# Optimization experiments

Hardware: AMD Instinct MI355X
Metric: run time of the kernel (lower is better)

## Reference

```python
import jax, jax.numpy as jnp
import numpy as np

B, S, IN, H, L = 512, 1024, 64, 32, 4


def setup_inputs() -> dict:
    key = jax.random.key(0)
    ks = jax.random.split(key, 9)
    s = 1.0 / np.sqrt(H)  # PyTorch RNN/Linear init scale
    u = lambda k, shape: jax.random.uniform(k, shape, jnp.float32, -s, s)
    return {
        "x": jax.random.normal(ks[0], (B, S, IN), jnp.float32),
        "h_state": jnp.zeros((L, B, H), jnp.float32),
        "W_ih0": u(ks[1], (H, IN)),          # layer 0 input weights
        "W_ih_rest": u(ks[2], (L - 1, H, H)),  # layers 1..3 input weights
        "W_hh": u(ks[3], (L, H, H)),
        "b_ih": u(ks[4], (L, H)),
        "b_hh": u(ks[5], (L, H)),
        "fc_w": u(ks[6], (1, H)),
        "fc_b": u(ks[7], (1,)),
    }


def _rnn_layer(seq_sbf, h0, W_ih, W_hh, b):
    # seq_sbf: [S, B, F]; vanilla RNN: h_t = tanh(x_t W_ih^T + h_{t-1} W_hh^T + b)
    def step(h, x_t):
        h = jnp.tanh(x_t @ W_ih.T + h @ W_hh.T + b)
        return h, h
    return jax.lax.scan(step, h0, seq_sbf)


def reference(x, h_state, W_ih0, W_ih_rest, W_hh, b_ih, b_hh, fc_w, fc_b):
    seq = jnp.swapaxes(x, 0, 1)  # [S, B, IN]
    h_finals = []
    for l in range(L):  # fixed small layer count
        W_ih = W_ih0 if l == 0 else W_ih_rest[l - 1]
        h_last, seq = _rnn_layer(seq, h_state[l], W_ih, W_hh[l], b_ih[l] + b_hh[l])
        h_finals.append(h_last)
    r_out = jnp.swapaxes(seq, 0, 1)                 # [B, S, H]
    logits = (r_out @ fc_w.T + fc_b)[..., 0]        # fused per-timestep Linear -> [B, S]
    probs = jax.nn.softmax(logits, axis=-1)         # nn.Softmax over last (seq) dim
    return probs, jnp.stack(h_finals, axis=0)       # [B,S], [L,B,H]
```

## Files before the change

kernel.cpp:

```cpp
#include <hip/hip_runtime.h>


#define BB 512
#define SS 1024
#define INF 64
#define HH 32
#define LL 4

typedef __fp16 v2h __attribute__((ext_vector_type(2)));

__device__ __forceinline__ v2h bch(unsigned u) { return __builtin_bit_cast(v2h, u); }
__device__ __forceinline__ unsigned bcu(v2h h) { return __builtin_bit_cast(unsigned, h); }

template <int CTRL>
__device__ __forceinline__ float dpp_add(float v) {
  int y = __builtin_amdgcn_update_dpp(0, __float_as_int(v), CTRL, 0xF, 0xF, true);
  return v + __int_as_float(y);
}
template <int CTRL>
__device__ __forceinline__ float dpp_mov(float v) {
  int y = __builtin_amdgcn_update_dpp(0, __float_as_int(v), CTRL, 0xF, 0xF, true);
  return __int_as_float(y);
}

__device__ __forceinline__ float tanh_fast(float a) {
  const float e = __builtin_amdgcn_exp2f(a * 2.885390081777927f);
  const float r = __builtin_amdgcn_rcpf(e + 1.0f);
  return __builtin_fmaf(-2.0f, r, 1.0f);
}

__device__ __forceinline__ float dot16v(const v2h* w, uint4 u0, uint4 u1) {
  float a = 0.f, c = 0.f;
  a = __builtin_amdgcn_fdot2(w[0], bch(u0.x), a, false);
  c = __builtin_amdgcn_fdot2(w[1], bch(u0.y), c, false);
  a = __builtin_amdgcn_fdot2(w[2], bch(u0.z), a, false);
  c = __builtin_amdgcn_fdot2(w[3], bch(u0.w), c, false);
  a = __builtin_amdgcn_fdot2(w[4], bch(u1.x), a, false);
  c = __builtin_amdgcn_fdot2(w[5], bch(u1.y), c, false);
  a = __builtin_amdgcn_fdot2(w[6], bch(u1.z), a, false);
  c = __builtin_amdgcn_fdot2(w[7], bch(u1.w), c, false);
  return a + c;
}

#define BAR() asm volatile("s_waitcnt lgkmcnt(0)\n\ts_barrier" ::: "memory")

__global__ __launch_bounds__(256) void u0_kernel(
    const float* __restrict__ x, const float* __restrict__ W_ih0,
    const float* __restrict__ b_ih, const float* __restrict__ b_hh,
    float* __restrict__ u0) {
  __shared__ float Wl[HH * INF];
  __shared__ float bl[HH];
  const int tid = threadIdx.x;
  {
    const float4* src = (const float4*)W_ih0;
    float4* dst = (float4*)Wl;
    dst[tid] = src[tid];
    dst[tid + 256] = src[tid + 256];
    if (tid < HH) bl[tid] = b_ih[tid] + b_hh[tid];
  }
  __syncthreads();

  const int row = blockIdx.x * 256 + tid;
  const float4* xr = (const float4*)(x + (size_t)row * INF);
  float acc[HH];
#pragma unroll
  for (int u = 0; u < HH; ++u) acc[u] = bl[u];
#pragma unroll 4
  for (int kc = 0; kc < 16; ++kc) {
    const float4 xv = xr[kc];
#pragma unroll
    for (int u = 0; u < HH; ++u) {
      const float4 wv = ((const float4*)Wl)[u * 16 + kc];
      acc[u] += wv.x * xv.x + wv.y * xv.y + wv.z * xv.z + wv.w * xv.w;
    }
  }
  float4* op = (float4*)(u0 + (size_t)row * HH);
#pragma unroll
  for (int j = 0; j < 8; ++j)
    op[j] = make_float4(acc[4 * j], acc[4 * j + 1], acc[4 * j + 2], acc[4 * j + 3]);
}

__global__ __launch_bounds__(256, 2) void rnn_kernel(
    const float* __restrict__ u0g_all, const float* __restrict__ h_state,
    const float* __restrict__ W_ih_rest, const float* __restrict__ W_hh,
    const float* __restrict__ b_ih, const float* __restrict__ b_hh,
    const float* __restrict__ fc_w, const float* __restrict__ fc_b,
    float* __restrict__ out) {
  __shared__ int hb[LL][2][2][16];
  __shared__ float h3f[2][2][32];
  __shared__ float lbuf[64];

  const int tid  = threadIdx.x;
  const int wid  = tid >> 6;
  const int lane = tid & 63;
  const int b    = blockIdx.x;
  const int ks   = lane & 1;
  const int h    = lane >> 1;

  v2h wih[8], whh[8];
  {
    const float2* ph = (const float2*)(W_hh + (size_t)(wid * HH + h) * HH + ks * 16);
#pragma unroll
    for (int j = 0; j < 8; ++j) whh[j] = __builtin_amdgcn_cvt_pkrtz(ph[j].x, ph[j].y);
  }
  float bias = 0.f;
  if (wid > 0) {
    const float2* pi =
        (const float2*)(W_ih_rest + (size_t)((wid - 1) * HH + h) * HH + ks * 16);
#pragma unroll
    for (int j = 0; j < 8; ++j) wih[j] = __builtin_amdgcn_cvt_pkrtz(pi[j].x, pi[j].y);
    bias = b_ih[wid * HH + h] + b_hh[wid * HH + h];
  }
  const float fcwh = fc_w[h] * 0.5f;
  const float fcb  = fc_b[0];

  if (lane < 16) {
    float a = h_state[(size_t)(wid * BB + b) * HH + 2 * lane];
    float c = h_state[(size_t)(wid * BB + b) * HH + 2 * lane + 1];
    hb[wid][(wid + 1) & 1][1][lane] = (int)bcu(__builtin_amdgcn_cvt_pkrtz(a, c));
  }

  const float* ug = u0g_all + (size_t)b * SS * HH;
  float ur[8];
  if (wid == 0) {
#pragma unroll
    for (int i = 0; i < 8; ++i) ur[i] = ug[i * HH + h];
  }
  float* const outrow = out + (size_t)b * SS;
  float* const hfin   = out + (size_t)BB * SS;

  __syncthreads();

  auto ld2 = [&](const int* p, uint4& A, uint4& B) __attribute__((always_inline)) {
    const uint4* q = (const uint4*)p;
    A = q[0]; B = q[1];
  };
  auto store_h = [&](int l, int buf, int slot, float hv) __attribute__((always_inline)) {
    float partner = dpp_mov<0xEE>(hv);
    if ((lane & 3) == 0)
      hb[l][buf][slot][lane >> 2] = (int)bcu(__builtin_amdgcn_cvt_pkrtz(hv, partner));
  };
  auto fcred = [&](float v) __attribute__((always_inline)) {
    v = dpp_add<0x111>(v);
    v = dpp_add<0x112>(v);
    v = dpp_add<0x114>(v);
    v = dpp_add<0x118>(v);
    v = dpp_add<0x142>(v);
    v = dpp_add<0x143>(v);
    return v;
  };

  if (wid == 0) {
    for (int n0 = 0; n0 < 516; n0 += 4) {
#pragma unroll
      for (int j = 0; j < 4; ++j) {
        BAR();
        const int n = n0 + j;
        const int buf = n & 1;
        if (n < 512) {
          uint4 Ha, Hb;
          ld2(&hb[0][buf ^ 1][1][ks * 8], Ha, Hb);
          float acc0 = dot16v(whh, Ha, Hb);
          acc0 = dpp_add<0xB1>(acc0) + ur[2 * j];
          const float hv0 = tanh_fast(acc0);
          store_h(0, buf, 0, hv0);
          uint4 Ga, Gb;
          ld2(&hb[0][buf][0][ks * 8], Ga, Gb);
          float acc1 = dot16v(whh, Ga, Gb);
          acc1 = dpp_add<0xB1>(acc1) + ur[2 * j + 1];
          const float hv1 = tanh_fast(acc1);
          store_h(0, buf, 1, hv1);
          if (n == 511 && ks == 0) hfin[(0 * BB + b) * HH + h] = hv1;
          int ta = 2 * n + 8; ta = ta < SS ? ta : SS - 1;
          int tb = 2 * n + 9; tb = tb < SS ? tb : SS - 1;
          ur[2 * j]     = ug[ta * HH + h];
          ur[2 * j + 1] = ug[tb * HH + h];
        }
        if (n >= 4) {
          const int tf = 2 * n - 7;
          float v0 = fcred(h3f[buf ^ 1][0][h] * fcwh);
          float v1 = fcred(h3f[buf ^ 1][1][h] * fcwh);
          if (lane == 63) {
            lbuf[(tf - 1) & 63] = v0 + fcb;
            lbuf[tf & 63]       = v1 + fcb;
          }
          if ((tf & 63) == 63) {
            float lv = lbuf[lane];
            outrow[tf - 63 + lane] = lv;
          }
        }
      }
    }
  } else if (wid < 3) {
    for (int n0 = 0; n0 < 516; n0 += 4) {
#pragma unroll
      for (int j = 0; j < 4; ++j) {
        BAR();
        const int n = n0 + j;
        const int buf = n & 1;
        if (n >= wid && n < 512 + wid) {
          uint4 I0a, I0b, I1a, I1b, Ha, Hb;
          ld2(&hb[wid - 1][buf ^ 1][0][ks * 8], I0a, I0b);
          ld2(&hb[wid - 1][buf ^ 1][1][ks * 8], I1a, I1b);
          ld2(&hb[wid][buf ^ 1][1][ks * 8], Ha, Hb);
          float acc0 = dot16v(wih, I0a, I0b) + dot16v(whh, Ha, Hb);
          acc0 = dpp_add<0xB1>(acc0) + bias;
          const float hv0 = tanh_fast(acc0);
          store_h(wid, buf, 0, hv0);
          uint4 Ga, Gb;
          ld2(&hb[wid][buf][0][ks * 8], Ga, Gb);
          float acc1 = dot16v(wih, I1a, I1b) + dot16v(whh, Ga, Gb);
          acc1 = dpp_add<0xB1>(acc1) + bias;
          const float hv1 = tanh_fast(acc1);
          store_h(wid, buf, 1, hv1);
          if (n == 511 + wid && ks == 0) hfin[(wid * BB + b) * HH + h] = hv1;
        }
      }
    }
  } else {
    for (int n0 = 0; n0 < 516; n0 += 4) {
#pragma unroll
      for (int j = 0; j < 4; ++j) {
        BAR();
        const int n = n0 + j;
        const int buf = n & 1;
        if (n >= 3 && n < 515) {
          uint4 I0a, I0b, I1a, I1b, Ha, Hb;
          ld2(&hb[2][buf ^ 1][0][ks * 8], I0a, I0b);
          ld2(&hb[2][buf ^ 1][1][ks * 8], I1a, I1b);
          ld2(&hb[3][buf ^ 1][1][ks * 8], Ha, Hb);
          float acc0 = dot16v(wih, I0a, I0b) + dot16v(whh, Ha, Hb);
          acc0 = dpp_add<0xB1>(acc0) + bias;
          const float hv0 = tanh_fast(acc0);
          store_h(3, buf, 0, hv0);
          if (ks == 0) h3f[buf][0][h] = hv0;
          uint4 Ga, Gb;
          ld2(&hb[3][buf][0][ks * 8], Ga, Gb);
          float acc1 = dot16v(wih, I1a, I1b) + dot16v(whh, Ga, Gb);
          acc1 = dpp_add<0xB1>(acc1) + bias;
          const float hv1 = tanh_fast(acc1);
          store_h(3, buf, 1, hv1);
          if (ks == 0) h3f[buf][1][h] = hv1;
          if (n == 514 && ks == 0) hfin[(3 * BB + b) * HH + h] = hv1;
        }
      }
    }
  }
}

__global__ __launch_bounds__(256) void softmax_kernel(float* __restrict__ out) {
  __shared__ float red[8];
  const int row = blockIdx.x;
  float* p = out + (size_t)row * SS;
  const int tid = threadIdx.x;
  float4 v = ((const float4*)p)[tid];
  float m = fmaxf(fmaxf(v.x, v.y), fmaxf(v.z, v.w));
#pragma unroll
  for (int d = 32; d >= 1; d >>= 1) m = fmaxf(m, __shfl_xor(m, d));
  if ((tid & 63) == 0) red[tid >> 6] = m;
  __syncthreads();
  m = fmaxf(fmaxf(red[0], red[1]), fmaxf(red[2], red[3]));
  const float e0 = __expf(v.x - m), e1 = __expf(v.y - m);
  const float e2 = __expf(v.z - m), e3 = __expf(v.w - m);
  float s = (e0 + e1) + (e2 + e3);
#pragma unroll
  for (int d = 32; d >= 1; d >>= 1) s += __shfl_xor(s, d);
  if ((tid & 63) == 0) red[4 + (tid >> 6)] = s;
  __syncthreads();
  s = (red[4] + red[5]) + (red[6] + red[7]);
  const float inv = 1.0f / s;
  float4 o;
  o.x = e0 * inv; o.y = e1 * inv; o.z = e2 * inv; o.w = e3 * inv;
  ((float4*)p)[tid] = o;
}

extern "C" void kernel_launch(void* const* d_in, const int* in_sizes, int n_in,
                              void* d_out, int out_size, void* d_ws, size_t ws_size,
                              hipStream_t stream) {
  const float* x         = (const float*)d_in[0];
  const float* h_state   = (const float*)d_in[1];
  const float* W_ih0     = (const float*)d_in[2];
  const float* W_ih_rest = (const float*)d_in[3];
  const float* W_hh      = (const float*)d_in[4];
  const float* b_ih      = (const float*)d_in[5];
  const float* b_hh      = (const float*)d_in[6];
  const float* fc_w      = (const float*)d_in[7];
  const float* fc_b      = (const float*)d_in[8];
  float* out = (float*)d_out;
  float* u0  = (float*)d_ws;

  hipLaunchKernelGGL(u0_kernel, dim3((BB * SS) / 256), dim3(256), 0, stream,
                     x, W_ih0, b_ih, b_hh, u0);
  hipLaunchKernelGGL(rnn_kernel, dim3(BB), dim3(256), 0, stream,
                     u0, h_state, W_ih_rest, W_hh, b_ih, b_hh, fc_w, fc_b, out);
  hipLaunchKernelGGL(softmax_kernel, dim3(BB), dim3(256), 0, stream, out);
}
```

Measured before the change: 457.0 us.

## Prefetch layer inputs a step early and keep recurrent state in registers

Each layer wave now loads its input from the previous layer one barrier step ahead into a double-buffered register array. Consequently the layer wavefront skew grows from one to two steps per layer, and the loop count, bounds and FC timestep offsets are adjusted to match. The second-slot hidden state is kept in registers (sv) and read right after storing, so the next step's critical path no longer waits on an LDS read. Initial state comes straight from global into registers, and the pre-loop __syncthreads is removed. This shortens the per-step dependency chain between barriers, at the cost of more registers and a few extra pipeline steps.

```diff
diff --git a/kernel.cpp b/kernel.cpp
--- a/kernel.cpp
+++ b/kernel.cpp
@@ -29,16 +29,13 @@
   return __builtin_fmaf(-2.0f, r, 1.0f);
 }
 
-__device__ __forceinline__ float dot16v(const v2h* w, uint4 u0, uint4 u1) {
+__device__ __forceinline__ float dot16p(const v2h* w, const v2h* v) {
   float a = 0.f, c = 0.f;
-  a = __builtin_amdgcn_fdot2(w[0], bch(u0.x), a, false);
-  c = __builtin_amdgcn_fdot2(w[1], bch(u0.y), c, false);
-  a = __builtin_amdgcn_fdot2(w[2], bch(u0.z), a, false);
-  c = __builtin_amdgcn_fdot2(w[3], bch(u0.w), c, false);
-  a = __builtin_amdgcn_fdot2(w[4], bch(u1.x), a, false);
-  c = __builtin_amdgcn_fdot2(w[5], bch(u1.y), c, false);
-  a = __builtin_amdgcn_fdot2(w[6], bch(u1.z), a, false);
-  c = __builtin_amdgcn_fdot2(w[7], bch(u1.w), c, false);
+#pragma unroll
+  for (int j = 0; j < 4; ++j) {
+    a = __builtin_amdgcn_fdot2(w[2 * j + 0], v[2 * j + 0], a, false);
+    c = __builtin_amdgcn_fdot2(w[2 * j + 1], v[2 * j + 1], c, false);
+  }
   return a + c;
 }
 
@@ -114,10 +111,12 @@
   const float fcwh = fc_w[h] * 0.5f;
   const float fcb  = fc_b[0];
 
-  if (lane < 16) {
-    float a = h_state[(size_t)(wid * BB + b) * HH + 2 * lane];
-    float c = h_state[(size_t)(wid * BB + b) * HH + 2 * lane + 1];
-    hb[wid][(wid + 1) & 1][1][lane] = (int)bcu(__builtin_amdgcn_cvt_pkrtz(a, c));
+  v2h sv[8];
+  {
+    const float2* hs = (const float2*)(h_state + (size_t)(wid * BB + b) * HH);
+#pragma unroll
+    for (int j = 0; j < 8; ++j)
+      sv[j] = __builtin_amdgcn_cvt_pkrtz(hs[ks * 8 + j].x, hs[ks * 8 + j].y);
   }
 
   const float* ug = u0g_all + (size_t)b * SS * HH;
@@ -129,11 +128,11 @@
   float* const outrow = out + (size_t)b * SS;
   float* const hfin   = out + (size_t)BB * SS;
 
-  __syncthreads();
-
-  auto ld2 = [&](const int* p, uint4& A, uint4& B) __attribute__((always_inline)) {
+  auto ld8 = [&](const int* p, v2h* v) __attribute__((always_inline)) {
     const uint4* q = (const uint4*)p;
-    A = q[0]; B = q[1];
+    uint4 A = q[0], B = q[1];
+    v[0] = bch(A.x); v[1] = bch(A.y); v[2] = bch(A.z); v[3] = bch(A.w);
+    v[4] = bch(B.x); v[5] = bch(B.y); v[6] = bch(B.z); v[7] = bch(B.w);
   };
   auto store_h = [&](int l, int buf, int slot, float hv) __attribute__((always_inline)) {
     float partner = dpp_mov<0xEE>(hv);
@@ -150,36 +149,43 @@
     return v;
   };
 
+  v2h vi[2][2][8];
+
   if (wid == 0) {
-    for (int n0 = 0; n0 < 516; n0 += 4) {
+    for (int n0 = 0; n0 < 520; n0 += 4) {
 #pragma unroll
       for (int j = 0; j < 4; ++j) {
         BAR();
         const int n = n0 + j;
-        const int buf = n & 1;
-        if (n < 512) {
-          uint4 Ha, Hb;
-          ld2(&hb[0][buf ^ 1][1][ks * 8], Ha, Hb);
-          float acc0 = dot16v(whh, Ha, Hb);
+        const int buf = j & 1;
+        float a0 = 0.f, a1 = 0.f;
+        const bool fc_on = (n >= 7 && n <= 518);
+        if (fc_on) {
+          a0 = h3f[buf ^ 1][0][h];
+          a1 = h3f[buf ^ 1][1][h];
+        }
+        if (n <= 511) {
+          float acc0 = dot16p(whh, sv);
           acc0 = dpp_add<0xB1>(acc0) + ur[2 * j];
           const float hv0 = tanh_fast(acc0);
           store_h(0, buf, 0, hv0);
-          uint4 Ga, Gb;
-          ld2(&hb[0][buf][0][ks * 8], Ga, Gb);
-          float acc1 = dot16v(whh, Ga, Gb);
+          v2h sv0[8];
+          ld8(&hb[0][buf][0][ks * 8], sv0);
+          float acc1 = dot16p(whh, sv0);
           acc1 = dpp_add<0xB1>(acc1) + ur[2 * j + 1];
           const float hv1 = tanh_fast(acc1);
           store_h(0, buf, 1, hv1);
+          ld8(&hb[0][buf][1][ks * 8], sv);
           if (n == 511 && ks == 0) hfin[(0 * BB + b) * HH + h] = hv1;
           int ta = 2 * n + 8; ta = ta < SS ? ta : SS - 1;
           int tb = 2 * n + 9; tb = tb < SS ? tb : SS - 1;
           ur[2 * j]     = ug[ta * HH + h];
           ur[2 * j + 1] = ug[tb * HH + h];
         }
-        if (n >= 4) {
-          const int tf = 2 * n - 7;
-          float v0 = fcred(h3f[buf ^ 1][0][h] * fcwh);
-          float v1 = fcred(h3f[buf ^ 1][1][h] * fcwh);
+        if (fc_on) {
+          const int tf = 2 * n - 13;
+          float v0 = fcred(a0 * fcwh);
+          float v1 = fcred(a1 * fcwh);
           if (lane == 63) {
             lbuf[(tf - 1) & 63] = v0 + fcb;
             lbuf[tf & 63]       = v1 + fcb;
@@ -192,56 +198,61 @@
       }
     }
   } else if (wid < 3) {
-    for (int n0 = 0; n0 < 516; n0 += 4) {
+    const int lo = 2 * wid, hi = 511 + 2 * wid;
+    for (int n0 = 0; n0 < 520; n0 += 4) {
 #pragma unroll
       for (int j = 0; j < 4; ++j) {
         BAR();
         const int n = n0 + j;
-        const int buf = n & 1;
-        if (n >= wid && n < 512 + wid) {
-          uint4 I0a, I0b, I1a, I1b, Ha, Hb;
-          ld2(&hb[wid - 1][buf ^ 1][0][ks * 8], I0a, I0b);
-          ld2(&hb[wid - 1][buf ^ 1][1][ks * 8], I1a, I1b);
-          ld2(&hb[wid][buf ^ 1][1][ks * 8], Ha, Hb);
-          float acc0 = dot16v(wih, I0a, I0b) + dot16v(whh, Ha, Hb);
+        const int buf = j & 1;
+        if (n >= lo - 1 && n <= hi - 1) {
+          ld8(&hb[wid - 1][buf ^ 1][0][ks * 8], vi[buf ^ 1][0]);
+          ld8(&hb[wid - 1][buf ^ 1][1][ks * 8], vi[buf ^ 1][1]);
+        }
+        if (n >= lo && n <= hi) {
+          float acc0 = dot16p(wih, vi[buf][0]) + dot16p(whh, sv);
           acc0 = dpp_add<0xB1>(acc0) + bias;
           const float hv0 = tanh_fast(acc0);
           store_h(wid, buf, 0, hv0);
-          uint4 Ga, Gb;
-          ld2(&hb[wid][buf][0][ks * 8], Ga, Gb);
-          float acc1 = dot16v(wih, I1a, I1b) + dot16v(whh, Ga, Gb);
+          v2h sv0[8];
+          ld8(&hb[wid][buf][0][ks * 8], sv0);
+          float acc1 = dot16p(wih, vi[buf][1]);
+          acc1 += dot16p(whh, sv0);
           acc1 = dpp_add<0xB1>(acc1) + bias;
           const float hv1 = tanh_fast(acc1);
           store_h(wid, buf, 1, hv1);
-          if (n == 511 + wid && ks == 0) hfin[(wid * BB + b) * HH + h] = hv1;
+          ld8(&hb[wid][buf][1][ks * 8], sv);
+          if (n == hi && ks == 0) hfin[(wid * BB + b) * HH + h] = hv1;
         }
       }
     }
   } else {
-    for (int n0 = 0; n0 < 516; n0 += 4) {
+    for (int n0 = 0; n0 < 520; n0 += 4) {
 #pragma unroll
       for (int j = 0; j < 4; ++j) {
         BAR();
         const int n = n0 + j;
-        const int buf = n & 1;
-        if (n >= 3 && n < 515) {
-          uint4 I0a, I0b, I1a, I1b, Ha, Hb;
-          ld2(&hb[2][buf ^ 1][0][ks * 8], I0a, I0b);
-          ld2(&hb[2][buf ^ 1][1][ks * 8], I1a, I1b);
-          ld2(&hb[3][buf ^ 1][1][ks * 8], Ha, Hb);
-          float acc0 = dot16v(wih, I0a, I0b) + dot16v(whh, Ha, Hb);
+        const int buf = j & 1;
+        if (n >= 5 && n <= 516) {
+          ld8(&hb[2][buf ^ 1][0][ks * 8], vi[buf ^ 1][0]);
+          ld8(&hb[2][buf ^ 1][1][ks * 8], vi[buf ^ 1][1]);
+        }
+        if (n >= 6 && n <= 517) {
+          float acc0 = dot16p(wih, vi[buf][0]) + dot16p(whh, sv);
           acc0 = dpp_add<0xB1>(acc0) + bias;
           const float hv0 = tanh_fast(acc0);
           store_h(3, buf, 0, hv0);
           if (ks == 0) h3f[buf][0][h] = hv0;
-          uint4 Ga, Gb;
-          ld2(&hb[3][buf][0][ks * 8], Ga, Gb);
-          float acc1 = dot16v(wih, I1a, I1b) + dot16v(whh, Ga, Gb);
+          v2h sv0[8];
+          ld8(&hb[3][buf][0][ks * 8], sv0);
+          float acc1 = dot16p(wih, vi[buf][1]);
+          acc1 += dot16p(whh, sv0);
           acc1 = dpp_add<0xB1>(acc1) + bias;
           const float hv1 = tanh_fast(acc1);
           store_h(3, buf, 1, hv1);
           if (ks == 0) h3f[buf][1][h] = hv1;
-          if (n == 514 && ks == 0) hfin[(3 * BB + b) * HH + h] = hv1;
+          ld8(&hb[3][buf][1][ks * 8], sv);
+          if (n == 517 && ks == 0) hfin[(3 * BB + b) * HH + h] = hv1;
         }
       }
     }
```

After: 456.9 us. About the same (-0.0%).
